# Optimization experiments

Hardware: AMD Instinct MI355X
Metric: run time of the kernel (lower is better)

Reference implementation:

```python
import jax, jax.numpy as jnp
import numpy as np
from functools import partial

B, S, H, L, NH, V, A, NL = 64, 256, 768, 12, 12, 30522, 64, 2
HD = H // NH
EPS = 1e-12


def _ln(x, s, b):
    m = jnp.mean(x, axis=-1, keepdims=True)
    v = jnp.mean((x - m) ** 2, axis=-1, keepdims=True)
    return (x - m) * jax.lax.rsqrt(v + EPS) * s + b


def setup_inputs() -> dict:
    key = jax.random.key(0)
    ks = jax.random.split(key, 16)
    sc = 0.02
    inp = {
        'input_ids': jax.random.randint(ks[0], (B, S), 0, V, dtype=jnp.int32),
        'attention_mask': jnp.ones((B, S), dtype=jnp.int32),
        'token_type_ids': jnp.zeros((B, S), dtype=jnp.int32),
        'annotator_idx': jax.random.randint(ks[1], (B,), 0, A, dtype=jnp.int32),
        'word_emb': jax.random.normal(ks[2], (V, H), jnp.float32) * sc,
        'pos_emb': jax.random.normal(ks[3], (512, H), jnp.float32) * sc,
        'type_emb': jax.random.normal(ks[4], (2, H), jnp.float32) * sc,
        'emb_ln_s': jnp.ones((H,), jnp.float32),
        'emb_ln_b': jnp.zeros((H,), jnp.float32),
        'Wq': jax.random.normal(ks[5], (L, H, H), jnp.float32) * sc,
        'bq': jnp.zeros((L, H), jnp.float32),
        'Wk': jax.random.normal(ks[6], (L, H, H), jnp.float32) * sc,
        'bk': jnp.zeros((L, H), jnp.float32),
        'Wv': jax.random.normal(ks[7], (L, H, H), jnp.float32) * sc,
        'bv': jnp.zeros((L, H), jnp.float32),
        'Wo': jax.random.normal(ks[8], (L, H, H), jnp.float32) * sc,
        'bo': jnp.zeros((L, H), jnp.float32),
        'ln1_s': jnp.ones((L, H), jnp.float32),
        'ln1_b': jnp.zeros((L, H), jnp.float32),
        'W1': jax.random.normal(ks[9], (L, H, 4 * H), jnp.float32) * sc,
        'b1': jnp.zeros((L, 4 * H), jnp.float32),
        'W2': jax.random.normal(ks[10], (L, 4 * H, H), jnp.float32) * sc,
        'b2': jnp.zeros((L, H), jnp.float32),
        'ln2_s': jnp.ones((L, H), jnp.float32),
        'ln2_b': jnp.zeros((L, H), jnp.float32),
        'head_W': jax.random.normal(ks[11], (A, H, NL), jnp.float32) * sc,
        'head_b': jnp.zeros((A, NL), jnp.float32),
    }
    return inp


def _bert_forward(input_ids, attention_mask, token_type_ids, word_emb, pos_emb,
                  type_emb, emb_ln_s, emb_ln_b, layer_params):
    # embeddings
    h = word_emb[input_ids] + pos_emb[:S][None, :, :] + type_emb[token_type_ids]
    h = _ln(h, emb_ln_s, emb_ln_b)
    # additive attention bias from mask: [B,1,1,S]
    mask_bias = (1.0 - attention_mask.astype(h.dtype))[:, None, None, :] * -10000.0
    scale = 1.0 / np.sqrt(HD)

    def layer(h, p):
        Wq, bq, Wk, bk, Wv, bv, Wo, bo, l1s, l1b, W1, b1, W2, b2, l2s, l2b = p
        def heads(x, W, b):  # [B,S,H] -> [B,NH,S,HD]
            y = x @ W + b
            return y.reshape(B, S, NH, HD).transpose(0, 2, 1, 3)
        q = heads(h, Wq, bq)
        k = heads(h, Wk, bk)
        v = heads(h, Wv, bv)
        scores = jnp.einsum('bhqd,bhkd->bhqk', q, k) * scale + mask_bias
        attn = jax.nn.softmax(scores, axis=-1)
        ctx = jnp.einsum('bhqk,bhkd->bhqd', attn, v)
        ctx = ctx.transpose(0, 2, 1, 3).reshape(B, S, H)
        h = _ln(h + ctx @ Wo + bo, l1s, l1b)
        ffn = jax.nn.gelu(h @ W1 + b1, approximate=False) @ W2 + b2
        h = _ln(h + ffn, l2s, l2b)
        return h, None

    h, _ = jax.lax.scan(layer, h, layer_params)
    return h


def reference(input_ids, attention_mask, token_type_ids, annotator_idx,
              word_emb, pos_emb, type_emb, emb_ln_s, emb_ln_b,
              Wq, bq, Wk, bk, Wv, bv, Wo, bo, ln1_s, ln1_b,
              W1, b1, W2, b2, ln2_s, ln2_b, head_W, head_b):
    layer_params = (Wq, bq, Wk, bk, Wv, bv, Wo, bo, ln1_s, ln1_b,
                    W1, b1, W2, b2, ln2_s, ln2_b)
    h = _bert_forward(input_ids, attention_mask, token_type_ids, word_emb,
                      pos_emb, type_emb, emb_ln_s, emb_ln_b, layer_params)
    cls = h[:, 0, :]  # [B,H]
    # per-sample annotator-head routing: gather head weights, batched matvec
    logits = jnp.einsum('bh,bhl->bl', cls, head_W[annotator_idx]) + head_b[annotator_idx]
    return logits
```

## Files before the change

### kernel.cpp

```cpp
#include <hip/hip_runtime.h>

#define L_ 12
#define H_ 768
#define S_ 256
#define B_ 64
#define NH_ 12
#define HD_ 64
#define FF_ 3072
#define M_ (B_*S_)
#define QKVN (3*H_)

using bf16x8 = __attribute__((ext_vector_type(8))) __bf16;
using floatx4 = __attribute__((ext_vector_type(4))) float;

typedef const __attribute__((address_space(1))) void* gptr_t;
typedef __attribute__((address_space(3))) void* sptr_t;

__device__ __forceinline__ void async_copy16(const void* g, void* s) {
  __builtin_amdgcn_global_load_lds((gptr_t)g, (sptr_t)s, 16, 0, 0);
}

__device__ __forceinline__ unsigned short f2bf(float f) {
  unsigned int u = __float_as_uint(f);
  u += 0x7fffu + ((u >> 16) & 1u);
  return (unsigned short)(u >> 16);
}
__device__ __forceinline__ float bf2f(unsigned short s) {
  return __uint_as_float(((unsigned int)s) << 16);
}

__device__ __forceinline__ float gelu_f(float x) {
  float y = 0.7978845608f * (x + 0.044715f * x * x * x);
  float t = 1.0f - 2.0f / (1.0f + __expf(2.0f * y));
  return 0.5f * x * (1.0f + t);
}

__global__ __launch_bounds__(256) void transpose_bf16_kernel(
    const float* __restrict__ W, unsigned short* __restrict__ Wt, int K, int N) {
  __shared__ unsigned short t[64][65];
  const int n0 = blockIdx.x * 64, k0 = blockIdx.y * 64;
  const int tid = threadIdx.x;
#pragma unroll
  for (int p = 0; p < 16; ++p) {
    int idx = p * 256 + tid;
    int r = idx >> 6, c = idx & 63;
    t[r][c] = f2bf(W[(size_t)(k0 + r) * N + n0 + c]);
  }
  __syncthreads();
#pragma unroll
  for (int p = 0; p < 16; ++p) {
    int idx = p * 256 + tid;
    int r = idx >> 6, c = idx & 63;
    Wt[(size_t)(n0 + r) * K + k0 + c] = t[c][r];
  }
}

__global__ __launch_bounds__(256) void v_transpose_kernel(
    const unsigned short* __restrict__ qkv, unsigned short* __restrict__ vT) {
  const int st = blockIdx.x, bh = blockIdx.y;
  const int b = bh / NH_, nh = bh % NH_;
  __shared__ unsigned short t[64][65];
  const int tid = threadIdx.x;
  const int s0 = st * 64;
  const size_t rowbase = (size_t)b * S_ * QKVN + 2 * H_ + nh * 64;
#pragma unroll
  for (int p = 0; p < 16; ++p) {
    int idx = p * 256 + tid;
    int r = idx >> 6, c = idx & 63;
    t[r][c] = qkv[rowbase + (size_t)(s0 + r) * QKVN + c];
  }
  __syncthreads();
#pragma unroll
  for (int p = 0; p < 16; ++p) {
    int idx = p * 256 + tid;
    int r = idx >> 6, c = idx & 63;
    vT[((size_t)bh * 64 + r) * 256 + s0 + c] = t[c][r];
  }
}

__global__ __launch_bounds__(256) void qkv_bias_kernel(
    const float* __restrict__ bq, const float* __restrict__ bk,
    const float* __restrict__ bv, float* __restrict__ out) {
  int i = blockIdx.x * 256 + threadIdx.x;
  if (i >= L_ * QKVN) return;
  int l = i / QKVN, j = i % QKVN;
  float v;
  if (j < H_) v = bq[l * H_ + j];
  else if (j < 2 * H_) v = bk[l * H_ + j - H_];
  else v = bv[l * H_ + j - 2 * H_];
  out[i] = v;
}

__global__ __launch_bounds__(256) void embed_ln_kernel(
    const int* __restrict__ ids, const int* __restrict__ tts,
    const float* __restrict__ wemb, const float* __restrict__ pemb,
    const float* __restrict__ temb, const float* __restrict__ lns,
    const float* __restrict__ lnb, float* __restrict__ h,
    unsigned short* __restrict__ hbf) {
  const int tk = blockIdx.x;
  const int s = tk & (S_ - 1);
  const int tid = threadIdx.x;
  const int id = ids[tk];
  const int tt = tts[tk];
  float v[3];
#pragma unroll
  for (int i = 0; i < 3; ++i) {
    int j = tid + i * 256;
    v[i] = wemb[(size_t)id * H_ + j] + pemb[(size_t)s * H_ + j] + temb[(size_t)tt * H_ + j];
  }
  float sum = v[0] + v[1] + v[2];
  float ssq = v[0] * v[0] + v[1] * v[1] + v[2] * v[2];
#pragma unroll
  for (int off = 32; off; off >>= 1) {
    sum += __shfl_down(sum, off);
    ssq += __shfl_down(ssq, off);
  }
  __shared__ float rs[4], rq[4];
  const int lane = tid & 63, wid = tid >> 6;
  if (lane == 0) { rs[wid] = sum; rq[wid] = ssq; }
  __syncthreads();
  const float S = rs[0] + rs[1] + rs[2] + rs[3];
  const float Q = rq[0] + rq[1] + rq[2] + rq[3];
  const float mean = S * (1.0f / 768.0f);
  const float var = Q * (1.0f / 768.0f) - mean * mean;
  const float r = rsqrtf(var + 1e-12f);
#pragma unroll
  for (int i = 0; i < 3; ++i) {
    int j = tid + i * 256;
    float y = (v[i] - mean) * r * lns[j] + lnb[j];
    h[(size_t)tk * H_ + j] = y;
    hbf[(size_t)tk * H_ + j] = f2bf(y);
  }
}

__global__ __launch_bounds__(256) void residual_ln_kernel(
    const float* __restrict__ hin, const unsigned short* __restrict__ delta,
    const float* __restrict__ lns, const float* __restrict__ lnb,
    float* __restrict__ hout, unsigned short* __restrict__ hbf) {
  const int row = blockIdx.x;
  const int tid = threadIdx.x;
  float v[3];
#pragma unroll
  for (int i = 0; i < 3; ++i) {
    int j = tid + i * 256;
    v[i] = hin[(size_t)row * H_ + j] + bf2f(delta[(size_t)row * H_ + j]);
  }
  float sum = v[0] + v[1] + v[2];
  float ssq = v[0] * v[0] + v[1] * v[1] + v[2] * v[2];
#pragma unroll
  for (int off = 32; off; off >>= 1) {
    sum += __shfl_down(sum, off);
    ssq += __shfl_down(ssq, off);
  }
  __shared__ float rs[4], rq[4];
  const int lane = tid & 63, wid = tid >> 6;
  if (lane == 0) { rs[wid] = sum; rq[wid] = ssq; }
  __syncthreads();
  const float S = rs[0] + rs[1] + rs[2] + rs[3];
  const float Q = rq[0] + rq[1] + rq[2] + rq[3];
  const float mean = S * (1.0f / 768.0f);
  const float var = Q * (1.0f / 768.0f) - mean * mean;
  const float r = rsqrtf(var + 1e-12f);
#pragma unroll
  for (int i = 0; i < 3; ++i) {
    int j = tid + i * 256;
    float y = (v[i] - mean) * r * lns[j] + lnb[j];
    hout[(size_t)row * H_ + j] = y;
    hbf[(size_t)row * H_ + j] = f2bf(y);
  }
}

enum { EPI_BF16 = 0, EPI_GELU = 1, EPI_F32 = 2 };

#define BAR() asm volatile("s_barrier" ::: "memory")
#define WAIT_LGKM0() do { asm volatile("s_waitcnt lgkmcnt(0)" ::: "memory"); \
                          __builtin_amdgcn_sched_barrier(0); } while (0)
#define VM_WAIT(n) asm volatile("s_waitcnt vmcnt(" #n ")" ::: "memory")

#define GEMM128_TILE(T_, SLOT_, NSLOT_, DOSTAGE_, VMASM_)                      \
  {                                                                            \
    const unsigned short* Ab_ = &AS[(SLOT_) * 4096];                           \
    const unsigned short* Bb_ = &BS[(SLOT_) * 4096];                           \
    bf16x8 af_[4], bf_[4];                                                     \
    _Pragma("unroll") for (int i_ = 0; i_ < 4; ++i_)                           \
        af_[i_] = *(const bf16x8*)(Ab_ + aoff + i_ * 512);                     \
    _Pragma("unroll") for (int j_ = 0; j_ < 4; ++j_)                           \
        bf_[j_] = *(const bf16x8*)(Bb_ + boff + j_ * 512);                     \
    if (DOSTAGE_) {                                                            \
      const unsigned short* ga_ = agp + (size_t)((T_) + 2) * 32;               \
      const unsigned short* gb_ = bgp + (size_t)((T_) + 2) * 32;               \
      _Pragma("unroll") for (int u_ = 0; u_ < 2; ++u_) {                       \
        async_copy16(ga_ + (size_t)u_ * 64 * K, asw + (NSLOT_) * 4096 + u_ * 2048); \
        async_copy16(gb_ + (size_t)u_ * 64 * K, bsw + (NSLOT_) * 4096 + u_ * 2048); \
      }                                                                        \
    }                                                                          \
    VMASM_;                                                                    \
    BAR();                                                                     \
    WAIT_LGKM0();                                                              \
    __builtin_amdgcn_s_setprio(1);                                             \
    _Pragma("unroll") for (int i_ = 0; i_ < 4; ++i_)                           \
      _Pragma("unroll") for (int j_ = 0; j_ < 4; ++j_)                         \
        acc[i_][j_] = __builtin_amdgcn_mfma_f32_16x16x32_bf16(                 \
            bf_[j_], af_[i_], acc[i_][j_], 0, 0, 0);                           \
    __builtin_amdgcn_s_setprio(0);                                             \
    BAR();                                                                     \
  }

template <int EPI>
__global__ __launch_bounds__(256, 3) void gemm128p_kernel(
    const unsigned short* __restrict__ A, const unsigned short* __restrict__ Bt,
    const float* __restrict__ bias, void* __restrict__ Cv,
    int M, int N, int K) {
  __shared__ __align__(128) unsigned short AS[3 * 4096];
  __shared__ __align__(128) unsigned short BS[3 * 4096];
  (void)M;
  const int NT = K >> 5;

  const int nwg = (int)gridDim.x;
  const int nbx = N >> 7;
  const int cpx = nwg >> 3;
  const int bid = (int)blockIdx.x;
  const int swz = (bid & 7) * cpx + (bid >> 3);
  const int n0 = (swz % nbx) << 7;
  const int m0 = (swz / nbx) << 7;

  const int tid = threadIdx.x;
  const int wave = tid >> 6;
  const int lane = tid & 63;
  const int lr = lane & 15;
  const int quad = lane >> 4;
  const int wgm = wave & 1;
  const int wgn = wave >> 1;

  const int colx = (quad ^ ((lr >> 1) & 3)) * 8;
  const int aoff = (wgm * 64 + lr) * 32 + colx;
  const int boff = (wgn * 64 + lr) * 32 + colx;

  const int srow = wave * 16 + (lane >> 2);
  const int scol = ((lane & 3) ^ ((lane >> 3) & 3)) * 8;
  const unsigned short* __restrict__ agp = A + (size_t)(m0 + srow) * K + scol;
  const unsigned short* __restrict__ bgp = Bt + (size_t)(n0 + srow) * K + scol;
  unsigned short* asw = &AS[wave * 512];
  unsigned short* bsw = &BS[wave * 512];

  floatx4 acc[4][4] = {};

#pragma unroll
  for (int t0 = 0; t0 < 2; ++t0) {
    const unsigned short* ga = agp + (size_t)t0 * 32;
    const unsigned short* gb = bgp + (size_t)t0 * 32;
#pragma unroll
    for (int u = 0; u < 2; ++u) {
      async_copy16(ga + (size_t)u * 64 * K, asw + t0 * 4096 + u * 2048);
      async_copy16(gb + (size_t)u * 64 * K, bsw + t0 * 4096 + u * 2048);
    }
  }
  VM_WAIT(4);
  BAR();

  int sl = 0;
  int t = 0;
  for (; t < NT - 2; ++t) {
    const int ns = (sl >= 1) ? sl - 1 : 2;
    GEMM128_TILE(t, sl, ns, true, VM_WAIT(4));
    sl = (sl == 2) ? 0 : sl + 1;
  }
  GEMM128_TILE(t, sl, 0, false, VM_WAIT(0));
  sl = (sl == 2) ? 0 : sl + 1;
  ++t;
  GEMM128_TILE(t, sl, 0, false, (void)0);

#pragma unroll
  for (int j = 0; j < 4; ++j) {
    const int nb = n0 + wgn * 64 + j * 16 + quad * 4;
    const float4 bv = *(const float4*)&bias[nb];
#pragma unroll
    for (int i = 0; i < 4; ++i) {
      const int m = m0 + wgm * 64 + i * 16 + lr;
      float v0 = acc[i][j][0] + bv.x;
      float v1 = acc[i][j][1] + bv.y;
      float v2 = acc[i][j][2] + bv.z;
      float v3 = acc[i][j][3] + bv.w;
      if (EPI == EPI_GELU) {
        v0 = gelu_f(v0); v1 = gelu_f(v1); v2 = gelu_f(v2); v3 = gelu_f(v3);
      }
      if (EPI == EPI_F32) {
        float4 o = make_float4(v0, v1, v2, v3);
        *(float4*)&((float*)Cv)[(size_t)m * N + nb] = o;
      } else {
        uint2 o;
        o.x = (unsigned)f2bf(v0) | ((unsigned)f2bf(v1) << 16);
        o.y = (unsigned)f2bf(v2) | ((unsigned)f2bf(v3) << 16);
        *(uint2*)&((unsigned short*)Cv)[(size_t)m * N + nb] = o;
      }
    }
  }
}

__global__ __launch_bounds__(256, 2) void flash_attn_kernel(
    const unsigned short* __restrict__ qkv, const unsigned short* __restrict__ vT,
    const int* __restrict__ mask, unsigned short* __restrict__ ctx) {
  const int bh = blockIdx.x;
  const int b = bh / NH_, nh = bh % NH_;
  __shared__ __align__(16) unsigned short Ks[64 * 64];
  __shared__ __align__(16) unsigned short Vs[64 * 64];
  __shared__ __align__(16) unsigned short Ps[4][64 * 66];
  __shared__ float bias_s[256];
  const int tid = threadIdx.x;
  const int wave = tid >> 6, lane = tid & 63;
  const int lr = lane & 15, quad = lane >> 4;
  bias_s[tid] = (1.0f - (float)mask[b * S_ + tid]) * -10000.0f;

  const size_t rowbase = (size_t)b * S_ * QKVN;
  const int q0 = wave * 64;

  bf16x8 qf[4][2];
#pragma unroll
  for (int i = 0; i < 4; ++i)
#pragma unroll
    for (int kc = 0; kc < 2; ++kc)
      qf[i][kc] = *(const bf16x8*)&qkv[rowbase + (size_t)(q0 + i * 16 + lr) * QKVN +
                                       nh * 64 + kc * 32 + quad * 8];

  floatx4 o[4][4] = {};
  float mrow[4][4], lrow[4][4];
#pragma unroll
  for (int i = 0; i < 4; ++i)
#pragma unroll
    for (int r = 0; r < 4; ++r) { mrow[i][r] = -1e30f; lrow[i][r] = 0.f; }

  const size_t vbase = (size_t)bh * 64 * 256;

  for (int jt = 0; jt < S_; jt += 64) {
    __syncthreads();
#pragma unroll
    for (int p = 0; p < 2; ++p) {
      int cid = p * 256 + wave * 64 + lane;
      int row = cid >> 3, c = cid & 7;
      async_copy16(&qkv[rowbase + (size_t)(jt + row) * QKVN + H_ + nh * 64 + c * 8],
                   &Ks[(p * 256 + wave * 64) * 8]);
      async_copy16(&vT[vbase + (size_t)row * 256 + jt + c * 8],
                   &Vs[(p * 256 + wave * 64) * 8]);
    }
    __syncthreads();

    floatx4 s[4][4];
#pragma unroll
    for (int jn = 0; jn < 4; ++jn) {
      bf16x8 kf0 = *(const bf16x8*)&Ks[(jn * 16 + lr) * 64 + quad * 8];
      bf16x8 kf1 = *(const bf16x8*)&Ks[(jn * 16 + lr) * 64 + 32 + quad * 8];
#pragma unroll
      for (int i = 0; i < 4; ++i) {
        floatx4 a = {};
        a = __builtin_amdgcn_mfma_f32_16x16x32_bf16(qf[i][0], kf0, a, 0, 0, 0);
        a = __builtin_amdgcn_mfma_f32_16x16x32_bf16(qf[i][1], kf1, a, 0, 0, 0);
        s[i][jn] = a;
      }
    }
    float bj[4];
#pragma unroll
    for (int jn = 0; jn < 4; ++jn) bj[jn] = bias_s[jt + jn * 16 + lr];
#pragma unroll
    for (int i = 0; i < 4; ++i)
#pragma unroll
      for (int jn = 0; jn < 4; ++jn)
#pragma unroll
        for (int r = 0; r < 4; ++r)
          s[i][jn][r] = s[i][jn][r] * 0.125f + bj[jn];

#pragma unroll
    for (int i = 0; i < 4; ++i) {
#pragma unroll
      for (int r = 0; r < 4; ++r) {
        float mx = fmaxf(fmaxf(s[i][0][r], s[i][1][r]), fmaxf(s[i][2][r], s[i][3][r]));
        mx = fmaxf(mx, __shfl_xor(mx, 1));
        mx = fmaxf(mx, __shfl_xor(mx, 2));
        mx = fmaxf(mx, __shfl_xor(mx, 4));
        mx = fmaxf(mx, __shfl_xor(mx, 8));
        float mn = fmaxf(mrow[i][r], mx);
        float alpha = __expf(mrow[i][r] - mn);
        mrow[i][r] = mn;
        float ps = 0.f;
#pragma unroll
        for (int jn = 0; jn < 4; ++jn) {
          float pv = __expf(s[i][jn][r] - mn);
          s[i][jn][r] = pv;
          ps += pv;
        }
        ps += __shfl_xor(ps, 1);
        ps += __shfl_xor(ps, 2);
        ps += __shfl_xor(ps, 4);
        ps += __shfl_xor(ps, 8);
        lrow[i][r] = lrow[i][r] * alpha + ps;
#pragma unroll
        for (int n = 0; n < 4; ++n) o[i][n][r] *= alpha;
      }
    }

#pragma unroll
    for (int i = 0; i < 4; ++i)
#pragma unroll
      for (int jn = 0; jn < 4; ++jn)
#pragma unroll
        for (int r = 0; r < 4; ++r)
          Ps[wave][(i * 16 + quad * 4 + r) * 66 + jn * 16 + lr] = f2bf(s[i][jn][r]);
    __syncthreads();

#pragma unroll
    for (int kc = 0; kc < 2; ++kc) {
      bf16x8 pf[4], vf[4];
#pragma unroll
      for (int i = 0; i < 4; ++i)
        pf[i] = *(const bf16x8*)&Ps[wave][(i * 16 + lr) * 66 + kc * 32 + quad * 8];
#pragma unroll
      for (int n = 0; n < 4; ++n)
        vf[n] = *(const bf16x8*)&Vs[(n * 16 + lr) * 64 + kc * 32 + quad * 8];
#pragma unroll
      for (int i = 0; i < 4; ++i)
#pragma unroll
        for (int n = 0; n < 4; ++n)
          o[i][n] = __builtin_amdgcn_mfma_f32_16x16x32_bf16(pf[i], vf[n], o[i][n], 0, 0, 0);
    }
  }

#pragma unroll
  for (int i = 0; i < 4; ++i) {
#pragma unroll
    for (int r = 0; r < 4; ++r) {
      float inv = 1.0f / lrow[i][r];
      int row = b * S_ + q0 + i * 16 + quad * 4 + r;
#pragma unroll
      for (int n = 0; n < 4; ++n)
        ctx[(size_t)row * H_ + nh * 64 + n * 16 + lr] = f2bf(o[i][n][r] * inv);
    }
  }
}

__global__ __launch_bounds__(256) void head_kernel(
    const float* __restrict__ h, const int* __restrict__ aidx,
    const float* __restrict__ hW, const float* __restrict__ hb,
    float* __restrict__ out) {
  const int b = blockIdx.x;
  const int a = aidx[b];
  const float* cls = h + (size_t)b * S_ * H_;
  const float* w = hW + (size_t)a * H_ * 2;
  float a0 = 0.f, a1 = 0.f;
  for (int j = threadIdx.x; j < H_; j += 256) {
    float c = cls[j];
    a0 += c * w[j * 2];
    a1 += c * w[j * 2 + 1];
  }
#pragma unroll
  for (int off = 32; off; off >>= 1) {
    a0 += __shfl_down(a0, off);
    a1 += __shfl_down(a1, off);
  }
  __shared__ float r0[4], r1[4];
  const int lane = threadIdx.x & 63, wid = threadIdx.x >> 6;
  if (lane == 0) { r0[wid] = a0; r1[wid] = a1; }
  __syncthreads();
  if (threadIdx.x == 0) {
    out[b * 2 + 0] = r0[0] + r0[1] + r0[2] + r0[3] + hb[a * 2 + 0];
    out[b * 2 + 1] = r1[0] + r1[1] + r1[2] + r1[3] + hb[a * 2 + 1];
  }
}

extern "C" void kernel_launch(void* const* d_in, const int* in_sizes, int n_in,
                              void* d_out, int out_size, void* d_ws, size_t ws_size,
                              hipStream_t stream) {
  const int* input_ids = (const int*)d_in[0];
  const int* attn_mask = (const int*)d_in[1];
  const int* type_ids = (const int*)d_in[2];
  const int* aidx = (const int*)d_in[3];
  const float* wemb = (const float*)d_in[4];
  const float* pemb = (const float*)d_in[5];
  const float* temb = (const float*)d_in[6];
  const float* elns = (const float*)d_in[7];
  const float* elnb = (const float*)d_in[8];
  const float* Wq = (const float*)d_in[9];
  const float* bq = (const float*)d_in[10];
  const float* Wk = (const float*)d_in[11];
  const float* bk = (const float*)d_in[12];
  const float* Wv = (const float*)d_in[13];
  const float* bv = (const float*)d_in[14];
  const float* Wo = (const float*)d_in[15];
  const float* bo = (const float*)d_in[16];
  const float* ln1s = (const float*)d_in[17];
  const float* ln1b = (const float*)d_in[18];
  const float* W1 = (const float*)d_in[19];
  const float* b1 = (const float*)d_in[20];
  const float* W2 = (const float*)d_in[21];
  const float* b2 = (const float*)d_in[22];
  const float* ln2s = (const float*)d_in[23];
  const float* ln2b = (const float*)d_in[24];
  const float* hW = (const float*)d_in[25];
  const float* hb = (const float*)d_in[26];
  float* out = (float*)d_out;
  (void)in_sizes; (void)n_in; (void)out_size; (void)ws_size;

  char* p = (char*)d_ws;
  float* h = (float*)p;              p += (size_t)M_ * H_ * 4;
  unsigned short* delta = (unsigned short*)p;  p += (size_t)M_ * H_ * 4;
  unsigned short* hbf = (unsigned short*)p;   p += (size_t)M_ * H_ * 2;
  unsigned short* qkv = (unsigned short*)p;   p += (size_t)M_ * QKVN * 2;
  unsigned short* ctx = (unsigned short*)p;   p += (size_t)M_ * H_ * 2;
  unsigned short* ffn1 = qkv;
  unsigned short* wbuf = (unsigned short*)p;  p += (size_t)7077888 * 2;
  float* qkvbias = (float*)p;        p += (size_t)L_ * QKVN * 4;
  unsigned short* vT = delta;

  unsigned short* Wqkv_t = wbuf;
  unsigned short* Wo_t = wbuf + (size_t)QKVN * H_;
  unsigned short* W1_t = Wo_t + (size_t)H_ * H_;
  unsigned short* W2_t = W1_t + (size_t)H_ * FF_;

  qkv_bias_kernel<<<(L_ * QKVN + 255) / 256, 256, 0, stream>>>(bq, bk, bv, qkvbias);
  embed_ln_kernel<<<M_, 256, 0, stream>>>(input_ids, type_ids, wemb, pemb, temb,
                                          elns, elnb, h, hbf);

  for (int l = 0; l < L_; ++l) {
    const size_t HH = (size_t)H_ * H_;
    const size_t HF = (size_t)H_ * FF_;
    transpose_bf16_kernel<<<dim3(12, 12), 256, 0, stream>>>(Wq + l * HH, Wqkv_t, H_, H_);
    transpose_bf16_kernel<<<dim3(12, 12), 256, 0, stream>>>(Wk + l * HH, Wqkv_t + HH, H_, H_);
    transpose_bf16_kernel<<<dim3(12, 12), 256, 0, stream>>>(Wv + l * HH, Wqkv_t + 2 * HH, H_, H_);
    transpose_bf16_kernel<<<dim3(12, 12), 256, 0, stream>>>(Wo + l * HH, Wo_t, H_, H_);
    transpose_bf16_kernel<<<dim3(48, 12), 256, 0, stream>>>(W1 + l * HF, W1_t, H_, FF_);
    transpose_bf16_kernel<<<dim3(12, 48), 256, 0, stream>>>(W2 + l * HF, W2_t, FF_, H_);

    gemm128p_kernel<EPI_BF16><<<dim3((QKVN / 128) * (M_ / 128)), 256, 0, stream>>>(
        hbf, Wqkv_t, qkvbias + (size_t)l * QKVN, qkv, M_, QKVN, H_);
    v_transpose_kernel<<<dim3(4, B_ * NH_), 256, 0, stream>>>(qkv, vT);
    flash_attn_kernel<<<B_ * NH_, 256, 0, stream>>>(qkv, vT, attn_mask, ctx);
    gemm128p_kernel<EPI_BF16><<<dim3((H_ / 128) * (M_ / 128)), 256, 0, stream>>>(
        ctx, Wo_t, bo + (size_t)l * H_, delta, M_, H_, H_);
    residual_ln_kernel<<<M_, 256, 0, stream>>>(h, delta, ln1s + (size_t)l * H_,
                                               ln1b + (size_t)l * H_, h, hbf);
    gemm128p_kernel<EPI_GELU><<<dim3((FF_ / 128) * (M_ / 128)), 256, 0, stream>>>(
        hbf, W1_t, b1 + (size_t)l * FF_, ffn1, M_, FF_, H_);
    gemm128p_kernel<EPI_BF16><<<dim3((H_ / 128) * (M_ / 128)), 256, 0, stream>>>(
        ffn1, W2_t, b2 + (size_t)l * H_, delta, M_, H_, FF_);
    residual_ln_kernel<<<M_, 256, 0, stream>>>(h, delta, ln2s + (size_t)l * H_,
                                               ln2b + (size_t)l * H_, h, hbf);
  }

  head_kernel<<<B_, 256, 0, stream>>>(h, aidx, hW, hb, out);
}
```

Baseline: 5.830 ms.

## Double-buffer GEMM register fragments with 4-slot LDS ring and merge weight transposes

Reworks the GEMM main loop so LDS fragment reads for the next k-tile are issued before the MFMAs of the current tile. It uses two register fragment sets and a 4-slot LDS ring, which drops one barrier per tile and overlaps LDS latency with compute. LDS use rises and launch bounds drop from 3 to 2 blocks per CU, so occupancy falls and register pressure rises. It also merges the six per-layer weight transpose launches into a single launch to cut launch overhead.

```diff
diff --git a/kernel.cpp b/kernel.cpp
--- a/kernel.cpp
+++ b/kernel.cpp
@@ -35,23 +35,47 @@
   return 0.5f * x * (1.0f + t);
 }
 
-__global__ __launch_bounds__(256) void transpose_bf16_kernel(
-    const float* __restrict__ W, unsigned short* __restrict__ Wt, int K, int N) {
+__global__ __launch_bounds__(256) void transpose_all_kernel(
+    const float* __restrict__ Wq, const float* __restrict__ Wk,
+    const float* __restrict__ Wv, const float* __restrict__ Wo,
+    const float* __restrict__ W1, const float* __restrict__ W2,
+    unsigned short* __restrict__ Wqkv_t, unsigned short* __restrict__ Wo_t,
+    unsigned short* __restrict__ W1_t, unsigned short* __restrict__ W2_t,
+    int l) {
+  const size_t HH = (size_t)H_ * H_;
+  const size_t HF = (size_t)H_ * FF_;
+  const int bid = blockIdx.x;
+  const float* src; unsigned short* dst; int K, N, bx, by;
+  if (bid < 432) {
+    int m = bid / 144, idx = bid % 144;
+    src = (m == 0 ? Wq : m == 1 ? Wk : Wv) + l * HH;
+    dst = Wqkv_t + (size_t)m * HH;
+    K = H_; N = H_; bx = idx % 12; by = idx / 12;
+  } else if (bid < 576) {
+    int idx = bid - 432;
+    src = Wo + l * HH; dst = Wo_t; K = H_; N = H_; bx = idx % 12; by = idx / 12;
+  } else if (bid < 1152) {
+    int idx = bid - 576;
+    src = W1 + l * HF; dst = W1_t; K = H_; N = FF_; bx = idx % 48; by = idx / 48;
+  } else {
+    int idx = bid - 1152;
+    src = W2 + l * HF; dst = W2_t; K = FF_; N = H_; bx = idx % 12; by = idx / 12;
+  }
   __shared__ unsigned short t[64][65];
-  const int n0 = blockIdx.x * 64, k0 = blockIdx.y * 64;
+  const int n0 = bx * 64, k0 = by * 64;
   const int tid = threadIdx.x;
 #pragma unroll
   for (int p = 0; p < 16; ++p) {
-    int idx = p * 256 + tid;
-    int r = idx >> 6, c = idx & 63;
-    t[r][c] = f2bf(W[(size_t)(k0 + r) * N + n0 + c]);
+    int idx2 = p * 256 + tid;
+    int r = idx2 >> 6, c = idx2 & 63;
+    t[r][c] = f2bf(src[(size_t)(k0 + r) * N + n0 + c]);
   }
   __syncthreads();
 #pragma unroll
   for (int p = 0; p < 16; ++p) {
-    int idx = p * 256 + tid;
-    int r = idx >> 6, c = idx & 63;
-    Wt[(size_t)(n0 + r) * K + k0 + c] = t[c][r];
+    int idx2 = p * 256 + tid;
+    int r = idx2 >> 6, c = idx2 & 63;
+    dst[(size_t)(n0 + r) * K + k0 + c] = t[c][r];
   }
 }
 
@@ -173,46 +197,37 @@
 enum { EPI_BF16 = 0, EPI_GELU = 1, EPI_F32 = 2 };
 
 #define BAR() asm volatile("s_barrier" ::: "memory")
-#define WAIT_LGKM0() do { asm volatile("s_waitcnt lgkmcnt(0)" ::: "memory"); \
-                          __builtin_amdgcn_sched_barrier(0); } while (0)
 #define VM_WAIT(n) asm volatile("s_waitcnt vmcnt(" #n ")" ::: "memory")
 
-#define GEMM128_TILE(T_, SLOT_, NSLOT_, DOSTAGE_, VMASM_)                      \
-  {                                                                            \
-    const unsigned short* Ab_ = &AS[(SLOT_) * 4096];                           \
-    const unsigned short* Bb_ = &BS[(SLOT_) * 4096];                           \
-    bf16x8 af_[4], bf_[4];                                                     \
+#define STAGE2(GA_, GB_, SL_)                                                  \
+  { _Pragma("unroll") for (int u_ = 0; u_ < 2; ++u_) {                         \
+      async_copy16((GA_) + (size_t)u_ * 64 * K, asw + (SL_) * 4096 + u_ * 2048); \
+      async_copy16((GB_) + (size_t)u_ * 64 * K, bsw + (SL_) * 4096 + u_ * 2048); \
+    } }
+
+#define READ_FRAGS(SL_, AF_, BF_)                                              \
+  { const unsigned short* Ab_ = &AS[(SL_) * 4096];                             \
+    const unsigned short* Bb_ = &BS[(SL_) * 4096];                             \
     _Pragma("unroll") for (int i_ = 0; i_ < 4; ++i_)                           \
-        af_[i_] = *(const bf16x8*)(Ab_ + aoff + i_ * 512);                     \
+        AF_[i_] = *(const bf16x8*)(Ab_ + aoff + i_ * 512);                     \
     _Pragma("unroll") for (int j_ = 0; j_ < 4; ++j_)                           \
-        bf_[j_] = *(const bf16x8*)(Bb_ + boff + j_ * 512);                     \
-    if (DOSTAGE_) {                                                            \
-      const unsigned short* ga_ = agp + (size_t)((T_) + 2) * 32;               \
-      const unsigned short* gb_ = bgp + (size_t)((T_) + 2) * 32;               \
-      _Pragma("unroll") for (int u_ = 0; u_ < 2; ++u_) {                       \
-        async_copy16(ga_ + (size_t)u_ * 64 * K, asw + (NSLOT_) * 4096 + u_ * 2048); \
-        async_copy16(gb_ + (size_t)u_ * 64 * K, bsw + (NSLOT_) * 4096 + u_ * 2048); \
-      }                                                                        \
-    }                                                                          \
-    VMASM_;                                                                    \
-    BAR();                                                                     \
-    WAIT_LGKM0();                                                              \
-    __builtin_amdgcn_s_setprio(1);                                             \
+        BF_[j_] = *(const bf16x8*)(Bb_ + boff + j_ * 512); }
+
+#define MFMA16(AF_, BF_)                                                       \
+  { __builtin_amdgcn_s_setprio(1);                                             \
     _Pragma("unroll") for (int i_ = 0; i_ < 4; ++i_)                           \
       _Pragma("unroll") for (int j_ = 0; j_ < 4; ++j_)                         \
         acc[i_][j_] = __builtin_amdgcn_mfma_f32_16x16x32_bf16(                 \
-            bf_[j_], af_[i_], acc[i_][j_], 0, 0, 0);                           \
-    __builtin_amdgcn_s_setprio(0);                                             \
-    BAR();                                                                     \
-  }
+            BF_[j_], AF_[i_], acc[i_][j_], 0, 0, 0);                           \
+    __builtin_amdgcn_s_setprio(0); }
 
 template <int EPI>
-__global__ __launch_bounds__(256, 3) void gemm128p_kernel(
+__global__ __launch_bounds__(256, 2) void gemm128p_kernel(
     const unsigned short* __restrict__ A, const unsigned short* __restrict__ Bt,
     const float* __restrict__ bias, void* __restrict__ Cv,
     int M, int N, int K) {
-  __shared__ __align__(128) unsigned short AS[3 * 4096];
-  __shared__ __align__(128) unsigned short BS[3 * 4096];
+  __shared__ __align__(128) unsigned short AS[4 * 4096];
+  __shared__ __align__(128) unsigned short BS[4 * 4096];
   (void)M;
   const int NT = K >> 5;
 
@@ -244,31 +259,39 @@
   unsigned short* bsw = &BS[wave * 512];
 
   floatx4 acc[4][4] = {};
-
-#pragma unroll
-  for (int t0 = 0; t0 < 2; ++t0) {
-    const unsigned short* ga = agp + (size_t)t0 * 32;
-    const unsigned short* gb = bgp + (size_t)t0 * 32;
-#pragma unroll
-    for (int u = 0; u < 2; ++u) {
-      async_copy16(ga + (size_t)u * 64 * K, asw + t0 * 4096 + u * 2048);
-      async_copy16(gb + (size_t)u * 64 * K, bsw + t0 * 4096 + u * 2048);
-    }
-  }
+  bf16x8 afA[4], bfA[4], afB[4], bfB[4];
+
+  STAGE2(agp, bgp, 0);
+  STAGE2(agp + 32, bgp + 32, 1);
   VM_WAIT(4);
   BAR();
-
-  int sl = 0;
-  int t = 0;
-  for (; t < NT - 2; ++t) {
-    const int ns = (sl >= 1) ? sl - 1 : 2;
-    GEMM128_TILE(t, sl, ns, true, VM_WAIT(4));
-    sl = (sl == 2) ? 0 : sl + 1;
-  }
-  GEMM128_TILE(t, sl, 0, false, VM_WAIT(0));
-  sl = (sl == 2) ? 0 : sl + 1;
-  ++t;
-  GEMM128_TILE(t, sl, 0, false, (void)0);
+  READ_FRAGS(0, afA, bfA);
+
+  const unsigned short* gA = agp + 2 * 32;
+  const unsigned short* gB = bgp + 2 * 32;
+  int sl_r = 1, sl_s = 2;
+  const int pairs = (NT - 2) >> 1;
+  for (int p = 0; p < pairs; ++p) {
+    STAGE2(gA, gB, sl_s);
+    gA += 32; gB += 32; sl_s = (sl_s + 1) & 3;
+    VM_WAIT(4);
+    BAR();
+    READ_FRAGS(sl_r, afB, bfB);
+    sl_r = (sl_r + 1) & 3;
+    MFMA16(afA, bfA);
+    STAGE2(gA, gB, sl_s);
+    gA += 32; gB += 32; sl_s = (sl_s + 1) & 3;
+    VM_WAIT(4);
+    BAR();
+    READ_FRAGS(sl_r, afA, bfA);
+    sl_r = (sl_r + 1) & 3;
+    MFMA16(afB, bfB);
+  }
+  VM_WAIT(0);
+  BAR();
+  READ_FRAGS(sl_r, afB, bfB);
+  MFMA16(afA, bfA);
+  MFMA16(afB, bfB);
 
 #pragma unroll
   for (int j = 0; j < 4; ++j) {
@@ -519,14 +542,8 @@
                                           elns, elnb, h, hbf);
 
   for (int l = 0; l < L_; ++l) {
-    const size_t HH = (size_t)H_ * H_;
-    const size_t HF = (size_t)H_ * FF_;
-    transpose_bf16_kernel<<<dim3(12, 12), 256, 0, stream>>>(Wq + l * HH, Wqkv_t, H_, H_);
-    transpose_bf16_kernel<<<dim3(12, 12), 256, 0, stream>>>(Wk + l * HH, Wqkv_t + HH, H_, H_);
-    transpose_bf16_kernel<<<dim3(12, 12), 256, 0, stream>>>(Wv + l * HH, Wqkv_t + 2 * HH, H_, H_);
-    transpose_bf16_kernel<<<dim3(12, 12), 256, 0, stream>>>(Wo + l * HH, Wo_t, H_, H_);
-    transpose_bf16_kernel<<<dim3(48, 12), 256, 0, stream>>>(W1 + l * HF, W1_t, H_, FF_);
-    transpose_bf16_kernel<<<dim3(12, 48), 256, 0, stream>>>(W2 + l * HF, W2_t, FF_, H_);
+    transpose_all_kernel<<<1728, 256, 0, stream>>>(Wq, Wk, Wv, Wo, W1, W2,
+                                                   Wqkv_t, Wo_t, W1_t, W2_t, l);
 
     gemm128p_kernel<EPI_BF16><<<dim3((QKVN / 128) * (M_ / 128)), 256, 0, stream>>>(
         hbf, Wqkv_t, qkvbias + (size_t)l * QKVN, qkv, M_, QKVN, H_);
```

After: 6.014 ms. 1.03x slower.
